# Performance work log

Measured on AMD Instinct MI355X. Metric: run time of the kernel, lower is better.

Reference implementation:

```python
import jax, jax.numpy as jnp
import numpy as np

N_NODES = 100000
IN_DIM = 64
EMB_DIM = 128
N_EDGES = 1600000
BN_EPS = 1e-5
GIN_EPS = 0.0  # train_eps=False, default eps=0


def setup_inputs() -> dict:
    key = jax.random.key(0)
    ks = jax.random.split(key, 10)
    x = jax.random.normal(ks[0], (N_NODES, IN_DIM), dtype=jnp.float32)
    edge_index = jax.random.randint(ks[1], (2, N_EDGES), 0, N_NODES, dtype=jnp.int64)
    edge_attr = jax.random.normal(ks[2], (N_EDGES, 4), dtype=jnp.float32)  # unused by module
    edge_weight = jax.random.uniform(ks[3], (N_EDGES,), dtype=jnp.float32)
    # MLP params: Linear(in,emb) -> BN(emb) -> ReLU -> Linear(emb,emb)
    lim1 = 1.0 / np.sqrt(IN_DIM)
    W1 = jax.random.uniform(ks[4], (IN_DIM, EMB_DIM), minval=-lim1, maxval=lim1, dtype=jnp.float32)
    b1 = jax.random.uniform(ks[5], (EMB_DIM,), minval=-lim1, maxval=lim1, dtype=jnp.float32)
    gamma = jnp.ones((EMB_DIM,), dtype=jnp.float32)
    beta = jnp.zeros((EMB_DIM,), dtype=jnp.float32)
    lim2 = 1.0 / np.sqrt(EMB_DIM)
    W2 = jax.random.uniform(ks[6], (EMB_DIM, EMB_DIM), minval=-lim2, maxval=lim2, dtype=jnp.float32)
    b2 = jax.random.uniform(ks[7], (EMB_DIM,), minval=-lim2, maxval=lim2, dtype=jnp.float32)
    return {"x": x, "edge_index": edge_index, "edge_attr": edge_attr,
            "edge_weight": edge_weight, "W1": W1, "b1": b1,
            "gamma": gamma, "beta": beta, "W2": W2, "b2": b2}


def reference(x, edge_index, edge_attr, edge_weight, W1, b1, gamma, beta, W2, b2):
    src, dst = edge_index[0], edge_index[1]  # message from x[src] aggregated at dst
    msg = x[src] * edge_weight[:, None]                       # [E, in_dim] gather + scale
    agg = jax.ops.segment_sum(msg, dst, num_segments=x.shape[0])  # [N, in_dim] scatter-add
    out = agg + (1.0 + GIN_EPS) * x                           # GIN self term
    # MLP: Linear -> BatchNorm1d (training stats, biased var) -> ReLU -> Linear
    h = out @ W1 + b1                                         # [N, emb]
    mean = jnp.mean(h, axis=0)
    var = jnp.var(h, axis=0)
    h = (h - mean) * jax.lax.rsqrt(var + BN_EPS) * gamma + beta
    h = jax.nn.relu(h)
    return h @ W2 + b2
```

## Files before the change

kernel.cpp:

```cpp
#include <hip/hip_runtime.h>

#define N_NODES 100000
#define IN_DIM 64
#define EMB 128
#define N_EDGES 1600000
#define BN_EPS 1e-5f

#define NB 98
#define BCAP 18432
#define FA_THREADS 512
#define FA_EPT 16
#define FA_BLK (FA_THREADS * FA_EPT)
#define FA_GRID ((N_EDGES + FA_BLK - 1) / FA_BLK)

#define WS_GSUM     0
#define WS_GSUM2    512
#define WS_BCUR     1024
#define WS_ROWSTART 2048
#define WS_PAIRS    802304
#define WS_AGG      13602304
#define WS_DSTARR   39202304
#define WS_SWARR    46427648
#define WS_X16      WS_DSTARR
#define WS_ZERO_BYTES 2048

typedef _Float16 half8_t __attribute__((ext_vector_type(8)));
typedef _Float16 half4_t __attribute__((ext_vector_type(4)));
typedef float floatx4 __attribute__((ext_vector_type(4)));

__global__ __launch_bounds__(512) void fillA_kernel(
    const int* __restrict__ ei, const float* __restrict__ ew,
    int* __restrict__ bcur, int* __restrict__ dstArr, float2* __restrict__ swArr)
{
    __shared__ int cnt[NB], base[NB];
    const int tid = threadIdx.x;
    if (tid < NB) cnt[tid] = 0;
    __syncthreads();
    const int e0 = blockIdx.x * FA_BLK;
    int pk[FA_EPT];
    #pragma unroll
    for (int i = 0; i < FA_EPT; ++i) {
        int e = e0 + i * FA_THREADS + tid;
        pk[i] = -1;
        if (e < N_EDGES) {
            int d = ei[N_EDGES + e];
            int b = d >> 10;
            int pos = atomicAdd(&cnt[b], 1);
            pk[i] = (b << 13) | pos;
        }
    }
    __syncthreads();
    if (tid < NB) base[tid] = atomicAdd(&bcur[tid], cnt[tid]);
    __syncthreads();
    #pragma unroll
    for (int i = 0; i < FA_EPT; ++i) {
        int e = e0 + i * FA_THREADS + tid;
        if (pk[i] >= 0) {
            int b = pk[i] >> 13, pos = pk[i] & 8191;
            int idx = b * BCAP + base[b] + pos;
            dstArr[idx] = ei[N_EDGES + e];
            swArr[idx]  = make_float2(__int_as_float(ei[e]), ew[e]);
        }
    }
}

__global__ __launch_bounds__(1024) void fillB2_kernel(
    const int* __restrict__ bcur, const int* __restrict__ dstArr,
    const float2* __restrict__ swArr,
    int* __restrict__ rowstart, float2* __restrict__ pairs)
{
    __shared__ int cnt2[1024];
    __shared__ int pre[1024];
    __shared__ int sbk[128];
    const int g = blockIdx.x;
    const int tid = threadIdx.x;

    if (tid < 128) sbk[tid] = (tid < NB) ? bcur[tid] : 0;
    cnt2[tid] = 0;
    __syncthreads();
    for (int off = 1; off < 128; off <<= 1) {
        int v = 0;
        if (tid < 128 && tid >= off) v = sbk[tid - off];
        __syncthreads();
        if (tid < 128) sbk[tid] += v;
        __syncthreads();
    }
    const int bucketBase = (g > 0) ? sbk[g - 1] : 0;

    const int nE = bcur[g];
    const int segBase = g * BCAP;
    for (int j = tid; j < nE; j += 1024)
        atomicAdd(&cnt2[dstArr[segBase + j] & 1023], 1);
    __syncthreads();

    const int c = cnt2[tid];
    pre[tid] = c;
    __syncthreads();
    for (int off = 1; off < 1024; off <<= 1) {
        int v = (tid >= off) ? pre[tid - off] : 0;
        __syncthreads();
        pre[tid] += v;
        __syncthreads();
    }
    const int start = bucketBase + pre[tid] - c;
    const int node = g * 1024 + tid;
    if (node < N_NODES) rowstart[node] = start;
    if (node == N_NODES - 1) rowstart[N_NODES] = start + c;

    __syncthreads();
    cnt2[tid] = start;
    __syncthreads();
    #pragma unroll 4
    for (int j = tid; j < nE; j += 1024) {
        int d = dstArr[segBase + j];
        int p = atomicAdd(&cnt2[d & 1023], 1);
        pairs[p] = swArr[segBase + j];
    }
}

__global__ __launch_bounds__(256) void cvt_kernel(
    const float4* __restrict__ x4, ushort4* __restrict__ x16)
{
    int i = blockIdx.x * 256 + threadIdx.x;
    if (i >= N_NODES * IN_DIM / 4) return;
    float4 v = x4[i];
    ushort4 u;
    _Float16 a = (_Float16)v.x, b = (_Float16)v.y,
             c = (_Float16)v.z, d = (_Float16)v.w;
    u.x = *(unsigned short*)&a; u.y = *(unsigned short*)&b;
    u.z = *(unsigned short*)&c; u.w = *(unsigned short*)&d;
    x16[i] = u;
}

#define G_NPW 5
__global__ __launch_bounds__(256) void gather_kernel(
    const _Float16* __restrict__ x16,
    const int* __restrict__ rowstart,
    const float2* __restrict__ pairs,
    float* __restrict__ agg)
{
    const int tid  = threadIdx.x;
    const int lane = tid & 63;
    const int wid  = tid >> 6;
    const int e    = lane >> 4;
    const int f    = lane & 15;
    const half4_t* __restrict__ xv4 = (const half4_t*)x16;
    const int node0 = (blockIdx.x * 4 + wid) * G_NPW;

    for (int r = 0; r < G_NPW; ++r) {
        const int n  = node0 + r;
        const int jb = rowstart[n];
        const int je = rowstart[n + 1];
        float4 accA = make_float4(0.f, 0.f, 0.f, 0.f);
        float4 accB = make_float4(0.f, 0.f, 0.f, 0.f);
        for (int j0 = jb; j0 < je; j0 += 64) {
            const int cnt = min(64, je - j0);
            float2 p = (lane < cnt) ? pairs[j0 + lane] : make_float2(0.f, 0.f);
            int   psrc = __float_as_int(p.x);
            float pw   = p.y;
            const int nch = (cnt + 7) >> 3;
            #pragma unroll 4
            for (int c = 0; c < nch; ++c) {
                int   uA = __shfl(psrc, c * 8 + e);
                float wA = __shfl(pw,   c * 8 + e);
                int   uB = __shfl(psrc, c * 8 + 4 + e);
                float wB = __shfl(pw,   c * 8 + 4 + e);
                half4_t va = xv4[(size_t)(unsigned)uA * 16 + f];
                half4_t vb = xv4[(size_t)(unsigned)uB * 16 + f];
                accA.x += wA * (float)va[0]; accA.y += wA * (float)va[1];
                accA.z += wA * (float)va[2]; accA.w += wA * (float)va[3];
                accB.x += wB * (float)vb[0]; accB.y += wB * (float)vb[1];
                accB.z += wB * (float)vb[2]; accB.w += wB * (float)vb[3];
            }
        }
        float4 s = make_float4(accA.x + accB.x, accA.y + accB.y,
                               accA.z + accB.z, accA.w + accB.w);
        s.x += __shfl_xor(s.x, 16); s.y += __shfl_xor(s.y, 16);
        s.z += __shfl_xor(s.z, 16); s.w += __shfl_xor(s.w, 16);
        s.x += __shfl_xor(s.x, 32); s.y += __shfl_xor(s.y, 32);
        s.z += __shfl_xor(s.z, 32); s.w += __shfl_xor(s.w, 32);
        if (e == 0)
            *(float4*)&agg[(size_t)n * IN_DIM + f * 4] = s;
    }
}

#define GM_ITERS 5
#define GM_ROWS (32 * GM_ITERS)
__global__ __launch_bounds__(256) void gemv_kernel(
    const float* __restrict__ agg,
    const float* __restrict__ x,
    const float* __restrict__ W1,
    const float* __restrict__ b1,
    float* __restrict__ h,
    float* __restrict__ gsum, float* __restrict__ gsum2)
{
    __shared__ _Float16 Ah[32][72];
    __shared__ float redS[EMB], redQ[EMB];

    const int tid  = threadIdx.x;
    const int lane = tid & 63;
    const int wid  = tid >> 6;
    const int rg   = wid >> 1;
    const int ch   = wid & 1;
    const int c0w  = ch * 64;
    const int l15  = lane & 15;
    const int kb   = lane >> 4;

    half8_t Bf[4][2];
    #pragma unroll
    for (int ct = 0; ct < 4; ++ct)
        #pragma unroll
        for (int kc = 0; kc < 2; ++kc)
            #pragma unroll
            for (int i = 0; i < 8; ++i)
                Bf[ct][kc][i] = (_Float16)W1[(kc * 32 + kb * 8 + i) * EMB + ct * 16 + c0w + l15];
    float b1c[4];
    #pragma unroll
    for (int ct = 0; ct < 4; ++ct) b1c[ct] = b1[ct * 16 + c0w + l15];

    if (tid < EMB) { redS[tid] = 0.f; redQ[tid] = 0.f; }

    float sAcc[4] = {0.f, 0.f, 0.f, 0.f};
    float qAcc[4] = {0.f, 0.f, 0.f, 0.f};

    const int r0blk = blockIdx.x * GM_ROWS;
    for (int it = 0; it < GM_ITERS; ++it) {
        const int r0 = r0blk + it * 32;
        __syncthreads();
        #pragma unroll
        for (int i = 0; i < 2; ++i) {
            int j   = i * 256 + tid;
            int row = j >> 4;
            int c4  = (j & 15) * 4;
            float4 av = *(const float4*)&agg[(size_t)(r0 + row) * IN_DIM + c4];
            float4 xv = *(const float4*)&x[(size_t)(r0 + row) * IN_DIM + c4];
            Ah[row][c4 + 0] = (_Float16)(av.x + xv.x);
            Ah[row][c4 + 1] = (_Float16)(av.y + xv.y);
            Ah[row][c4 + 2] = (_Float16)(av.z + xv.z);
            Ah[row][c4 + 3] = (_Float16)(av.w + xv.w);
        }
        __syncthreads();

        floatx4 acc[4];
        #pragma unroll
        for (int ct = 0; ct < 4; ++ct)
            acc[ct] = (floatx4){b1c[ct], b1c[ct], b1c[ct], b1c[ct]};
        #pragma unroll
        for (int kc = 0; kc < 2; ++kc) {
            half8_t af = *(half8_t*)&Ah[rg * 16 + l15][kc * 32 + kb * 8];
            #pragma unroll
            for (int ct = 0; ct < 4; ++ct)
                acc[ct] = __builtin_amdgcn_mfma_f32_16x16x32_f16(af, Bf[ct][kc], acc[ct], 0, 0, 0);
        }

        #pragma unroll
        for (int ct = 0; ct < 4; ++ct) {
            #pragma unroll
            for (int i = 0; i < 4; ++i) {
                int row = r0 + rg * 16 + kb * 4 + i;
                float v = acc[ct][i];
                h[(size_t)row * EMB + c0w + ct * 16 + l15] = v;
                sAcc[ct] += v;
                qAcc[ct] += v * v;
            }
        }
    }

    __syncthreads();
    #pragma unroll
    for (int ct = 0; ct < 4; ++ct) {
        atomicAdd(&redS[c0w + ct * 16 + l15], sAcc[ct]);
        atomicAdd(&redQ[c0w + ct * 16 + l15], qAcc[ct]);
    }
    __syncthreads();
    if (tid < EMB) {
        atomicAdd(&gsum[tid],  redS[tid]);
        atomicAdd(&gsum2[tid], redQ[tid]);
    }
}

#define MR 32
#define M2_ITERS 5
#define M2_ROWS (MR * M2_ITERS)

__global__ __launch_bounds__(256) void mlp2_kernel(
    float* __restrict__ hio,
    const float* __restrict__ gsum, const float* __restrict__ gsum2,
    const float* __restrict__ gamma, const float* __restrict__ beta,
    const float* __restrict__ W2,
    const float* __restrict__ b2)
{
    __shared__ _Float16 Ph[MR][136];
    __shared__ float abuf[EMB], bbuf[EMB];

    const int tid  = threadIdx.x;
    const int lane = tid & 63;
    const int wid  = tid >> 6;
    const int rg   = wid >> 1;
    const int ch   = wid & 1;
    const int c0w  = ch * 64;
    const int l15  = lane & 15;
    const int kb   = lane >> 4;

    if (tid < EMB) {
        const float invN = 1.0f / (float)N_NODES;
        float mean = gsum[tid] * invN;
        float var  = gsum2[tid] * invN - mean * mean;
        float inv  = rsqrtf(var + BN_EPS);
        float a    = gamma[tid] * inv;
        abuf[tid] = a;
        bbuf[tid] = beta[tid] - mean * a;
    }

    const int bcol = c0w + l15;
    half8_t Bf[4][4];
    #pragma unroll
    for (int ct = 0; ct < 4; ++ct) {
        #pragma unroll
        for (int kc = 0; kc < 4; ++kc) {
            #pragma unroll
            for (int i = 0; i < 8; ++i)
                Bf[ct][kc][i] = (_Float16)W2[(kc * 32 + kb * 8 + i) * EMB + ct * 16 + bcol];
        }
    }
    float b2c[4];
    #pragma unroll
    for (int ct = 0; ct < 4; ++ct) b2c[ct] = b2[ct * 16 + bcol];

    __syncthreads();

    const int r0blk = blockIdx.x * M2_ROWS;
    for (int it = 0; it < M2_ITERS; ++it) {
        const int r0 = r0blk + it * MR;
        #pragma unroll
        for (int i = 0; i < 8; ++i) {
            int j   = i * 256 + tid;
            int row = j >> 6;
            int c2  = (j & 63) * 2;
            const float2 hv = *(const float2*)&hio[(size_t)(r0 + row) * EMB + c2];
            float p0 = fmaxf(hv.x * abuf[c2]     + bbuf[c2],     0.f);
            float p1 = fmaxf(hv.y * abuf[c2 + 1] + bbuf[c2 + 1], 0.f);
            Ph[row][c2]     = (_Float16)p0;
            Ph[row][c2 + 1] = (_Float16)p1;
        }
        __syncthreads();

        floatx4 acc[4];
        #pragma unroll
        for (int ct = 0; ct < 4; ++ct)
            acc[ct] = (floatx4){b2c[ct], b2c[ct], b2c[ct], b2c[ct]};
        #pragma unroll
        for (int kc = 0; kc < 4; ++kc) {
            half8_t af = *(half8_t*)&Ph[rg * 16 + l15][kc * 32 + kb * 8];
            #pragma unroll
            for (int ct = 0; ct < 4; ++ct)
                acc[ct] = __builtin_amdgcn_mfma_f32_16x16x32_f16(af, Bf[ct][kc], acc[ct], 0, 0, 0);
        }
        __syncthreads();

        #pragma unroll
        for (int ct = 0; ct < 4; ++ct) {
            #pragma unroll
            for (int i = 0; i < 4; ++i) {
                int row = r0 + rg * 16 + kb * 4 + i;
                hio[(size_t)row * EMB + c0w + ct * 16 + l15] = acc[ct][i];
            }
        }
    }
}

extern "C" void kernel_launch(void* const* d_in, const int* in_sizes, int n_in,
                              void* d_out, int out_size, void* d_ws, size_t ws_size,
                              hipStream_t stream)
{
    const float* x     = (const float*)d_in[0];
    const int*   ei    = (const int*)d_in[1];
    const float* ew    = (const float*)d_in[3];
    const float* W1    = (const float*)d_in[4];
    const float* b1    = (const float*)d_in[5];
    const float* gamma = (const float*)d_in[6];
    const float* beta  = (const float*)d_in[7];
    const float* W2    = (const float*)d_in[8];
    const float* b2    = (const float*)d_in[9];

    char* ws = (char*)d_ws;
    float*    gsum     = (float*)(ws + WS_GSUM);
    float*    gsum2    = (float*)(ws + WS_GSUM2);
    int*      bcur     = (int*)(ws + WS_BCUR);
    int*      rowstart = (int*)(ws + WS_ROWSTART);
    float2*   pairs    = (float2*)(ws + WS_PAIRS);
    float*    agg      = (float*)(ws + WS_AGG);
    int*      dstArr   = (int*)(ws + WS_DSTARR);
    float2*   swArr    = (float2*)(ws + WS_SWARR);
    _Float16* x16      = (_Float16*)(ws + WS_X16);
    float*    h        = (float*)d_out;

    hipMemsetAsync(d_ws, 0, WS_ZERO_BYTES, stream);

    fillA_kernel<<<FA_GRID, FA_THREADS, 0, stream>>>(ei, ew, bcur, dstArr, swArr);
    fillB2_kernel<<<NB, 1024, 0, stream>>>(bcur, dstArr, swArr, rowstart, pairs);
    cvt_kernel<<<(N_NODES * IN_DIM / 4 + 255) / 256, 256, 0, stream>>>(
        (const float4*)x, (ushort4*)x16);
    gather_kernel<<<N_NODES / (4 * G_NPW), 256, 0, stream>>>(x16, rowstart, pairs, agg);
    gemv_kernel<<<N_NODES / GM_ROWS, 256, 0, stream>>>(agg, x, W1, b1, h, gsum, gsum2);
    mlp2_kernel<<<N_NODES / M2_ROWS, 256, 0, stream>>>(h, gsum, gsum2, gamma, beta, W2, b2);
}
```

Baseline: 162.4 us.

## Restructure first MLP GEMM to per-wave 16-row tiles loaded directly into registers

Each wave now owns whole 16-row tiles covering all 128 output columns, and builds its MFMA A fragments straight from global agg and x instead of staging them through shared memory with block-wide barriers. The grid grows to many small blocks, each handling two tiles per wave, which is meant to raise parallelism and remove the LDS round trip and syncs. BatchNorm statistics are reduced with wave shuffles plus a small per-wave LDS array instead of shared-memory atomics. The cost is more registers per thread (16 B fragments, 8 accumulators) and duplicated W1 loads across many more blocks.

New measurement: 162.5 us. No clear change (+0.0%).

```diff
diff --git a/kernel.cpp b/kernel.cpp
--- a/kernel.cpp
+++ b/kernel.cpp
@@ -184,8 +184,9 @@
     }
 }
 
-#define GM_ITERS 5
-#define GM_ROWS (32 * GM_ITERS)
+#define GV_TPW 2
+#define GV_TILES (N_NODES / 16)
+#define GV_GRID ((GV_TILES + 4 * GV_TPW - 1) / (4 * GV_TPW))
 __global__ __launch_bounds__(256) void gemv_kernel(
     const float* __restrict__ agg,
     const float* __restrict__ x,
@@ -194,88 +195,90 @@
     float* __restrict__ h,
     float* __restrict__ gsum, float* __restrict__ gsum2)
 {
-    __shared__ _Float16 Ah[32][72];
-    __shared__ float redS[EMB], redQ[EMB];
+    __shared__ float redS[4][EMB], redQ[4][EMB];
 
     const int tid  = threadIdx.x;
     const int lane = tid & 63;
     const int wid  = tid >> 6;
-    const int rg   = wid >> 1;
-    const int ch   = wid & 1;
-    const int c0w  = ch * 64;
     const int l15  = lane & 15;
     const int kb   = lane >> 4;
 
-    half8_t Bf[4][2];
-    #pragma unroll
-    for (int ct = 0; ct < 4; ++ct)
+    half8_t Bf[8][2];
+    #pragma unroll
+    for (int ct = 0; ct < 8; ++ct)
         #pragma unroll
         for (int kc = 0; kc < 2; ++kc)
             #pragma unroll
             for (int i = 0; i < 8; ++i)
-                Bf[ct][kc][i] = (_Float16)W1[(kc * 32 + kb * 8 + i) * EMB + ct * 16 + c0w + l15];
-    float b1c[4];
-    #pragma unroll
-    for (int ct = 0; ct < 4; ++ct) b1c[ct] = b1[ct * 16 + c0w + l15];
-
-    if (tid < EMB) { redS[tid] = 0.f; redQ[tid] = 0.f; }
-
-    float sAcc[4] = {0.f, 0.f, 0.f, 0.f};
-    float qAcc[4] = {0.f, 0.f, 0.f, 0.f};
-
-    const int r0blk = blockIdx.x * GM_ROWS;
-    for (int it = 0; it < GM_ITERS; ++it) {
-        const int r0 = r0blk + it * 32;
-        __syncthreads();
-        #pragma unroll
-        for (int i = 0; i < 2; ++i) {
-            int j   = i * 256 + tid;
-            int row = j >> 4;
-            int c4  = (j & 15) * 4;
-            float4 av = *(const float4*)&agg[(size_t)(r0 + row) * IN_DIM + c4];
-            float4 xv = *(const float4*)&x[(size_t)(r0 + row) * IN_DIM + c4];
-            Ah[row][c4 + 0] = (_Float16)(av.x + xv.x);
-            Ah[row][c4 + 1] = (_Float16)(av.y + xv.y);
-            Ah[row][c4 + 2] = (_Float16)(av.z + xv.z);
-            Ah[row][c4 + 3] = (_Float16)(av.w + xv.w);
-        }
-        __syncthreads();
-
-        floatx4 acc[4];
-        #pragma unroll
-        for (int ct = 0; ct < 4; ++ct)
+                Bf[ct][kc][i] = (_Float16)W1[(kc * 32 + kb * 8 + i) * EMB + ct * 16 + l15];
+    float b1c[8];
+    #pragma unroll
+    for (int ct = 0; ct < 8; ++ct) b1c[ct] = b1[ct * 16 + l15];
+
+    float sA[8] = {0,0,0,0,0,0,0,0};
+    float qA[8] = {0,0,0,0,0,0,0,0};
+
+    #pragma unroll
+    for (int j = 0; j < GV_TPW; ++j) {
+        const int t = blockIdx.x * (4 * GV_TPW) + wid * GV_TPW + j;
+        if (t >= GV_TILES) break;
+        const size_t rowb = (size_t)(t * 16 + l15) * IN_DIM + kb * 8;
+        half8_t af[2];
+        #pragma unroll
+        for (int kc = 0; kc < 2; ++kc) {
+            float4 a0 = *(const float4*)(agg + rowb + kc * 32);
+            float4 a1 = *(const float4*)(agg + rowb + kc * 32 + 4);
+            float4 x0 = *(const float4*)(x   + rowb + kc * 32);
+            float4 x1 = *(const float4*)(x   + rowb + kc * 32 + 4);
+            af[kc][0] = (_Float16)(a0.x + x0.x);
+            af[kc][1] = (_Float16)(a0.y + x0.y);
+            af[kc][2] = (_Float16)(a0.z + x0.z);
+            af[kc][3] = (_Float16)(a0.w + x0.w);
+            af[kc][4] = (_Float16)(a1.x + x1.x);
+            af[kc][5] = (_Float16)(a1.y + x1.y);
+            af[kc][6] = (_Float16)(a1.z + x1.z);
+            af[kc][7] = (_Float16)(a1.w + x1.w);
+        }
+        floatx4 acc[8];
+        #pragma unroll
+        for (int ct = 0; ct < 8; ++ct)
             acc[ct] = (floatx4){b1c[ct], b1c[ct], b1c[ct], b1c[ct]};
         #pragma unroll
-        for (int kc = 0; kc < 2; ++kc) {
-            half8_t af = *(half8_t*)&Ah[rg * 16 + l15][kc * 32 + kb * 8];
-            #pragma unroll
-            for (int ct = 0; ct < 4; ++ct)
-                acc[ct] = __builtin_amdgcn_mfma_f32_16x16x32_f16(af, Bf[ct][kc], acc[ct], 0, 0, 0);
-        }
-
-        #pragma unroll
-        for (int ct = 0; ct < 4; ++ct) {
+        for (int kc = 0; kc < 2; ++kc)
+            #pragma unroll
+            for (int ct = 0; ct < 8; ++ct)
+                acc[ct] = __builtin_amdgcn_mfma_f32_16x16x32_f16(af[kc], Bf[ct][kc], acc[ct], 0, 0, 0);
+        #pragma unroll
+        for (int ct = 0; ct < 8; ++ct) {
             #pragma unroll
             for (int i = 0; i < 4; ++i) {
-                int row = r0 + rg * 16 + kb * 4 + i;
-                float v = acc[ct][i];
-                h[(size_t)row * EMB + c0w + ct * 16 + l15] = v;
-                sAcc[ct] += v;
-                qAcc[ct] += v * v;
+                const int r = t * 16 + kb * 4 + i;
+                const float v = acc[ct][i];
+                h[(size_t)r * EMB + ct * 16 + l15] = v;
+                sA[ct] += v;
+                qA[ct] += v * v;
             }
         }
     }
 
-    __syncthreads();
-    #pragma unroll
-    for (int ct = 0; ct < 4; ++ct) {
-        atomicAdd(&redS[c0w + ct * 16 + l15], sAcc[ct]);
-        atomicAdd(&redQ[c0w + ct * 16 + l15], qAcc[ct]);
+    #pragma unroll
+    for (int ct = 0; ct < 8; ++ct) {
+        sA[ct] += __shfl_xor(sA[ct], 16); sA[ct] += __shfl_xor(sA[ct], 32);
+        qA[ct] += __shfl_xor(qA[ct], 16); qA[ct] += __shfl_xor(qA[ct], 32);
+    }
+    if (lane < 16) {
+        #pragma unroll
+        for (int ct = 0; ct < 8; ++ct) {
+            redS[wid][ct * 16 + lane] = sA[ct];
+            redQ[wid][ct * 16 + lane] = qA[ct];
+        }
     }
     __syncthreads();
     if (tid < EMB) {
-        atomicAdd(&gsum[tid],  redS[tid]);
-        atomicAdd(&gsum2[tid], redQ[tid]);
+        float s = redS[0][tid] + redS[1][tid] + redS[2][tid] + redS[3][tid];
+        float q = redQ[0][tid] + redQ[1][tid] + redQ[2][tid] + redQ[3][tid];
+        atomicAdd(&gsum[tid],  s);
+        atomicAdd(&gsum2[tid], q);
     }
 }
 
@@ -402,6 +405,6 @@
     cvt_kernel<<<(N_NODES * IN_DIM / 4 + 255) / 256, 256, 0, stream>>>(
         (const float4*)x, (ushort4*)x16);
     gather_kernel<<<N_NODES / (4 * G_NPW), 256, 0, stream>>>(x16, rowstart, pairs, agg);
-    gemv_kernel<<<N_NODES / GM_ROWS, 256, 0, stream>>>(agg, x, W1, b1, h, gsum, gsum2);
+    gemv_kernel<<<GV_GRID, 256, 0, stream>>>(agg, x, W1, b1, h, gsum, gsum2);
     mlp2_kernel<<<N_NODES / M2_ROWS, 256, 0, stream>>>(h, gsum, gsum2, gamma, beta, W2, b2);
 }
```
